# Kernel tuning notes

Hardware: AMD Instinct MI355X
Metric: run time of the kernel (lower is better)

The kernel has to match this reference:

```python
import jax, jax.numpy as jnp
import numpy as np

B, S, T, L, D, H = 32, 64, 256, 8, 128, 128
SIGNAL_SD = 1.0 - 0.001   # default signal_sds init
NOISE_SD = 0.01           # GP diagonal jitter (noise_sds) for Cholesky stability


def setup_inputs() -> dict:
    key = jax.random.key(0)
    ks = jax.random.split(key, 8)
    X = jax.random.normal(ks[0], (B, T, D), dtype=jnp.float32)
    times = (jnp.arange(T, dtype=jnp.float32) / T) * 10.0  # span [0, 10)
    log_taus = jax.random.normal(ks[1], (L,), dtype=jnp.float32) * 0.1 + jnp.log(0.5)
    log_R_diag = jax.random.normal(ks[2], (D,), dtype=jnp.float32) * 0.1
    W1 = jax.random.normal(ks[3], (L, H), dtype=jnp.float32) / np.sqrt(L)
    b1 = jnp.zeros((H,), dtype=jnp.float32)
    W2 = jax.random.normal(ks[4], (H, D), dtype=jnp.float32) / np.sqrt(H)
    b2 = jnp.zeros((D,), dtype=jnp.float32)
    eps = jax.random.normal(ks[5], (B, S, L, T), dtype=jnp.float32)
    return {"X": X, "times": times, "log_taus": log_taus, "log_R_diag": log_R_diag,
            "W1": W1, "b1": b1, "W2": W2, "b2": b2, "eps": eps}


def reference(X, times, log_taus, log_R_diag, W1, b1, W2, b2, eps):
    taus = jnp.exp(log_taus)            # [L]
    r = jnp.exp(log_R_diag)             # [D] diagonal of R

    # --- GP prior kernel matrices (squared-exponential SDE kernel), one per latent dim ---
    dt = times[:, None] - times[None, :]                       # [T,T]
    K = (SIGNAL_SD ** 2) * jnp.exp(-(dt ** 2)[None] / (2.0 * (taus ** 2)[:, None, None]))
    K = K + (NOISE_SD ** 2) * jnp.eye(T, dtype=K.dtype)        # [L,T,T]
    Lc = jnp.linalg.cholesky(K)                                # [L,T,T]

    # --- reparameterized prior samples: z = Lc @ eps ---
    z = jnp.einsum('lut,bslt->bslu', Lc, eps)                  # [B,S,L,T]
    Z = jnp.transpose(z, (0, 1, 3, 2))                         # [B,S,T,L]

    # --- decoder MLP: latent -> manifold mean in observation space ---
    h = jnp.tanh(jnp.einsum('bstl,lh->bsth', Z, W1) + b1)      # [B,S,T,H]
    mu = jnp.einsum('bsth,hd->bstd', h, W2) + b2               # [B,S,T,D]

    # --- diagonal-R Gaussian log_prob per timestep, closed form ---
    diff = X[:, None, :, :] - mu                               # [B,S,T,D]
    quad = jnp.sum(diff * diff / r, axis=-1)                   # [B,S,T]
    log_norm = 0.5 * (jnp.sum(log_R_diag) + D * jnp.log(2.0 * jnp.pi))
    logp = -0.5 * quad - log_norm                              # [B,S,T]

    # --- sum over time, logsumexp over MC samples ---
    ll = jnp.sum(logp, axis=2)                                 # [B,S]
    nll = -(jax.scipy.special.logsumexp(ll, axis=1) - jnp.log(jnp.float32(S)))
    return nll                                                 # [B]
```

## Files before the change

kernel.cpp:

```cpp
#include <hip/hip_runtime.h>
#include <hip/hip_bf16.h>
#include <math.h>

#define B_ 32
#define S_ 64
#define T_ 256
#define L_ 8
#define D_ 128
#define H_ 128

typedef __attribute__((ext_vector_type(8))) short short8;
typedef __attribute__((ext_vector_type(4))) short short4v;
typedef __attribute__((ext_vector_type(4))) float float4v;

__device__ __forceinline__ short f2bf(float x) {
  __hip_bfloat16 h = __float2bfloat16(x);
  return *reinterpret_cast<short*>(&h);
}

__device__ __forceinline__ float rdlane(float x, int sl) {
  return __int_as_float(__builtin_amdgcn_readlane(__float_as_int(x), sl));
}
__device__ __forceinline__ float dpp_shr1(float x, float tailv) {
  int r = __builtin_amdgcn_update_dpp(__float_as_int(tailv), __float_as_int(x),
                                      0x138, 0xF, 0xF, false);
  return __int_as_float(r);
}

__global__ __launch_bounds__(64) void k_chol_prep(
    const float* __restrict__ times, const float* __restrict__ log_taus,
    __hip_bfloat16* __restrict__ Lcbf_,
    const float* __restrict__ W1, const float* __restrict__ W2,
    __hip_bfloat16* __restrict__ W1T, __hip_bfloat16* __restrict__ W2T)
{
  __shared__ short panel[256][68];
  const int bi = blockIdx.x;
  const int j = threadIdx.x;

  if (bi >= 8) {
    const int base = (bi - 8) * 64 + j;
    for (int idx = base; idx < H_ * D_; idx += 4096) {
      const int cc = idx >> 7, h = idx & 127;
      const int n = cc & 15, nt = cc >> 4;
      const int d = n * 8 + nt;
      W2T[(size_t)cc * H_ + h] = __float2bfloat16(W2[(size_t)h * D_ + d]);
    }
    for (int idx = base; idx < L_ * H_; idx += 4096) {
      const int li = idx >> 7, h = idx & 127;
      W1T[(size_t)h * L_ + li] = __float2bfloat16(W1[idx]);
    }
    return;
  }

  const int l = bi;
  short* Lbf = (short*)Lcbf_ + (size_t)l * T_ * T_;

  const float tau = expf(log_taus[l]);
  const float inv2tau2 = 0.5f / (tau * tau);
  const float sig2 = 0.999f * 0.999f;
  const float t0 = times[0];

  const float c0 = sig2 + 1e-4f;
  const float isc0 = 1.0f / sqrtf(c0);

  float u[4], v[4];
#pragma unroll
  for (int c = 0; c < 4; ++c) {
    const int d = c * 64 + j;
    const float dt = times[d] - t0;
    float cv = sig2 * __expf(-dt * dt * inv2tau2);
    if (d == 0) cv = c0;
    u[c] = cv * isc0;
    v[c] = (d == 0) ? 0.0f : u[c];
  }

#pragma unroll
  for (int p = 0; p < 4; ++p) {
    for (int kk = 0; kk < 64; ++kk) {
      const float uk = rdlane(u[p], kk);
      const float vk = rdlane(v[p], kk);
      const float rho = vk * __builtin_amdgcn_rcpf(uk);
      const float om = fmaxf(1.0f - rho * rho, 1e-12f);
      const float s = __builtin_amdgcn_rsqf(om);
      const float sr = s * rho;

      float up[4];
#pragma unroll
      for (int c = 0; c < 4; ++c) {
        if (c >= p) {
          const float uc = u[c], vc = v[c];
          up[c] = s * uc - sr * vc;
          v[c]  = s * vc - sr * uc;
          const float val = (c > p || j >= kk) ? up[c] : 0.0f;
          panel[(c - p) * 64 + j][kk] = f2bf(val);
        }
      }
#pragma unroll
      for (int c = 3; c >= 0; --c) {
        if (c >= p) {
          const float tail = (c > p) ? rdlane(up[c - 1], 63) : 0.0f;
          u[c] = dpp_shr1(up[c], tail);
        }
      }
    }
    __syncthreads();
    const int rpt = 256 - 64 * p;
    const int rsub = j >> 4, cp = (j & 15) * 4;
    for (int i0 = 0; i0 < rpt; i0 += 4) {
      const int pr = i0 + rsub;
      short4v vv = *(const short4v*)&panel[pr][cp];
      *(short4v*)&Lbf[((size_t)(p * 64 + pr) << 8) + p * 64 + cp] = vv;
    }
    __syncthreads();
  }
}

__global__ __launch_bounds__(256) void k_zgemm(
    const float* __restrict__ eps, const __hip_bfloat16* __restrict__ Lcbf_,
    __hip_bfloat16* __restrict__ Zg)
{
  __shared__ __align__(16) short E[64][264];
  const int bi = blockIdx.x;
  const int l = bi & 7, bs0 = (bi >> 3) * 64;
  const int tid = threadIdx.x, w = tid >> 6, lane = tid & 63;
  const int n = lane & 15, q = lane >> 4;
  const short* Lb = (const short*)Lcbf_ + (size_t)l * T_ * T_;

  {
    const int row = tid >> 2, seg = (tid & 3) * 64;
    const float* src = eps + ((size_t)(bs0 + row) * L_ + l) * T_ + seg;
#pragma unroll
    for (int g = 0; g < 16; ++g) {
      float4v f = *(const float4v*)(src + g * 4);
      short4v o;
#pragma unroll
      for (int jj = 0; jj < 4; ++jj) o[jj] = f2bf(f[jj]);
      *(short4v*)&E[row][seg + g * 4] = o;
    }
  }
  __syncthreads();

  float4v acc[4][4];
#pragma unroll
  for (int mt = 0; mt < 4; ++mt)
#pragma unroll
    for (int nt = 0; nt < 4; ++nt) acc[mt][nt] = (float4v){0.f, 0.f, 0.f, 0.f};

  const int kend = (w + 1) * 64;
  for (int k0 = 0; k0 < kend; k0 += 32) {
    short8 bfrg[4], afr[4];
#pragma unroll
    for (int nt = 0; nt < 4; ++nt)
      bfrg[nt] = *(const short8*)&E[nt * 16 + n][k0 + q * 8];
#pragma unroll
    for (int mt = 0; mt < 4; ++mt) {
      const int u = w * 64 + mt * 16 + n;
      afr[mt] = *(const short8*)&Lb[((size_t)u << 8) + k0 + q * 8];
    }
#pragma unroll
    for (int mt = 0; mt < 4; ++mt)
#pragma unroll
      for (int nt = 0; nt < 4; ++nt)
        acc[mt][nt] = __builtin_amdgcn_mfma_f32_16x16x32_bf16(afr[mt], bfrg[nt], acc[mt][nt], 0, 0, 0);
  }
#pragma unroll
  for (int mt = 0; mt < 4; ++mt)
#pragma unroll
    for (int nt = 0; nt < 4; ++nt) {
      const int bs = bs0 + nt * 16 + n;
#pragma unroll
      for (int r = 0; r < 4; ++r) {
        const int u = w * 64 + mt * 16 + q * 4 + r;
        Zg[((size_t)bs << 11) + (u << 3) + l] = __float2bfloat16(acc[mt][nt][r]);
      }
    }
}

__global__ __launch_bounds__(256, 4) void k_decode(
    const float* __restrict__ X, const __hip_bfloat16* __restrict__ Zg,
    const __hip_bfloat16* __restrict__ W1T, const float* __restrict__ b1,
    const __hip_bfloat16* __restrict__ W2T, const float* __restrict__ b2,
    const float* __restrict__ log_R, float* __restrict__ ll)
{
  __shared__ __align__(16) short Zt[256][8];
  __shared__ __align__(16) __hip_bfloat16 hS[128][136];
  __shared__ float redbuf[4];

  const int bs = blockIdx.x;
  const int b = bs >> 6;
  const int tid = threadIdx.x;
  const int w = tid >> 6, lane = tid & 63;
  const int n = lane & 15, q = lane >> 4;
  const short* Zs = (const short*)Zg;
  const short* W1s = (const short*)W1T;
  const short* W2s = (const short*)W2T;

  *(short8*)&Zt[tid][0] = *(const short8*)&Zs[((size_t)bs << 11) + tid * 8];

  float sLR = log_R[lane] + log_R[lane + 64];
#pragma unroll
  for (int off = 32; off >= 1; off >>= 1) sLR += __shfl_xor(sLR, off);

  const int d0 = n * 8 + 2 * w;
  float invr2[2], b22[2], b12[2];
#pragma unroll
  for (int jj = 0; jj < 2; ++jj) {
    invr2[jj] = expf(-log_R[d0 + jj]);
    b22[jj] = b2[d0 + jj];
    b12[jj] = b1[(2 * w + jj) * 16 + n];
  }

  const short8 zero8 = {0, 0, 0, 0, 0, 0, 0, 0};
  short8 w1f[2];
  short8 bfr[2][4];
#pragma unroll
  for (int jj = 0; jj < 2; ++jj) {
    const int c = (2 * w + jj) * 16 + n;
    short8 v = zero8;
    if (q == 0) v = *(const short8*)&W1s[(size_t)c * L_];
    w1f[jj] = v;
#pragma unroll
    for (int ks = 0; ks < 4; ++ks)
      bfr[jj][ks] = *(const short8*)&W2s[(size_t)c * H_ + ks * 32 + q * 8];
  }

  float qsum = 0.0f;
  __syncthreads();

#pragma unroll 1
  for (int half = 0; half < 2; ++half) {
#pragma unroll 1
    for (int mi = 0; mi < 8; ++mi) {
      short8 zf = zero8;
      if (q == 0) zf = *(const short8*)&Zt[half * 128 + mi * 16 + n][0];
      float4v c0 = __builtin_amdgcn_mfma_f32_16x16x32_bf16(zf, w1f[0], (float4v){0.f,0.f,0.f,0.f}, 0, 0, 0);
      float4v c1 = __builtin_amdgcn_mfma_f32_16x16x32_bf16(zf, w1f[1], (float4v){0.f,0.f,0.f,0.f}, 0, 0, 0);
#pragma unroll
      for (int r = 0; r < 4; ++r) {
        float a0 = c0[r] + b12[0];
        float a1 = c1[r] + b12[1];
        float p0 = __expf(2.f * a0) + 1.f;
        float p1 = __expf(2.f * a1) + 1.f;
        float rj = __builtin_amdgcn_rcpf(p0 * p1);
        float h0 = 1.f - 2.f * p1 * rj;
        float h1 = 1.f - 2.f * p0 * rj;
        hS[mi * 16 + q * 4 + r][(2 * w) * 16 + n] = __float2bfloat16(h0);
        hS[mi * 16 + q * 4 + r][(2 * w + 1) * 16 + n] = __float2bfloat16(h1);
      }
    }
    __syncthreads();
#pragma unroll 1
    for (int mi = 0; mi < 8; ++mi) {
      short8 af[4];
#pragma unroll
      for (int ks = 0; ks < 4; ++ks)
        af[ks] = *(const short8*)&hS[mi * 16 + n][ks * 32 + q * 8];
      float4v acc0 = (float4v){0.f, 0.f, 0.f, 0.f};
      float4v acc1 = (float4v){0.f, 0.f, 0.f, 0.f};
#pragma unroll
      for (int ks = 0; ks < 4; ++ks) {
        acc0 = __builtin_amdgcn_mfma_f32_16x16x32_bf16(af[ks], bfr[0][ks], acc0, 0, 0, 0);
        acc1 = __builtin_amdgcn_mfma_f32_16x16x32_bf16(af[ks], bfr[1][ks], acc1, 0, 0, 0);
      }
#pragma unroll
      for (int r = 0; r < 4; ++r) {
        const int t = half * 128 + mi * 16 + q * 4 + r;
        const float2 xv = *(const float2*)(X + (((size_t)b << 8) + t) * D_ + d0);
        float diff0 = xv.x - (acc0[r] + b22[0]);
        float diff1 = xv.y - (acc1[r] + b22[1]);
        qsum += diff0 * diff0 * invr2[0] + diff1 * diff1 * invr2[1];
      }
    }
    __syncthreads();
  }

#pragma unroll
  for (int off = 32; off >= 1; off >>= 1) qsum += __shfl_xor(qsum, off);
  if (lane == 0) redbuf[w] = qsum;
  __syncthreads();
  if (tid == 0) {
    float Q = redbuf[0] + redbuf[1] + redbuf[2] + redbuf[3];
    float log_norm = 0.5f * (sLR + (float)D_ * 1.8378770664093453f);
    ll[bs] = -0.5f * Q - (float)T_ * log_norm;
  }
}

__global__ __launch_bounds__(64) void k_lse(
    const float* __restrict__ ll, float* __restrict__ out)
{
  const int b = blockIdx.x;
  const int s = threadIdx.x;
  float v = ll[b * 64 + s];
  float m = v;
#pragma unroll
  for (int off = 32; off >= 1; off >>= 1) m = fmaxf(m, __shfl_xor(m, off));
  float e = __expf(v - m);
#pragma unroll
  for (int off = 32; off >= 1; off >>= 1) e += __shfl_xor(e, off);
  if (s == 0) out[b] = -(m + __logf(e) - 4.1588830833596715f);
}

extern "C" void kernel_launch(void* const* d_in, const int* in_sizes, int n_in,
                              void* d_out, int out_size, void* d_ws, size_t ws_size,
                              hipStream_t stream) {
  const float* X        = (const float*)d_in[0];
  const float* times    = (const float*)d_in[1];
  const float* log_taus = (const float*)d_in[2];
  const float* log_R    = (const float*)d_in[3];
  const float* W1       = (const float*)d_in[4];
  const float* b1       = (const float*)d_in[5];
  const float* W2       = (const float*)d_in[6];
  const float* b2       = (const float*)d_in[7];
  const float* eps      = (const float*)d_in[8];
  float* out = (float*)d_out;

  char* ws = (char*)d_ws;
  __hip_bfloat16* Lcbf = (__hip_bfloat16*)(ws);
  __hip_bfloat16* Zg   = (__hip_bfloat16*)(ws + 1048576);
  float* ll            = (float*)(ws + 9437184);
  __hip_bfloat16* W2T  = (__hip_bfloat16*)(ws + 9445376);
  __hip_bfloat16* W1T  = (__hip_bfloat16*)(ws + 9478144);

  hipLaunchKernelGGL(k_chol_prep, dim3(72),   dim3(64),  0, stream,
                     times, log_taus, Lcbf, W1, W2, W1T, W2T);
  hipLaunchKernelGGL(k_zgemm,     dim3(256),  dim3(256), 0, stream, eps, Lcbf, Zg);
  hipLaunchKernelGGL(k_decode,    dim3(2048), dim3(256), 0, stream, X, Zg, W1T, b1, W2T, b2, log_R, ll);
  hipLaunchKernelGGL(k_lse,       dim3(32),   dim3(64),  0, stream, ll, out);
}
```

Baseline: 174.2 us.

## Rebalance triangular zgemm tiles, change Z layout, shrink decode LDS and tweak math

The Z GEMM now uses 32-column blocks and pairs triangular row tiles per wave (w, 15-w, 7-w, 8+w), so each wave's work skipping zero blocks of the lower-triangular Cholesky factor is roughly equal. Its output is staged through LDS and written as coalesced L-major rows. The decode kernel gathers the per-latent values from that layout and processes four quarters with a smaller hS buffer, raising the occupancy hint to 7. Smaller edits permute the W1T columns so tanh pairs store as packed bf16x2, compute tanh through exp2 with folded constants, and simplify the Givens rotation in the Cholesky. The scattered 2-byte Z gathers in decode and the extra LDS pass in zgemm could cost more than the load balancing saves.

```diff
diff --git a/kernel.cpp b/kernel.cpp
--- a/kernel.cpp
+++ b/kernel.cpp
@@ -12,6 +12,7 @@
 typedef __attribute__((ext_vector_type(8))) short short8;
 typedef __attribute__((ext_vector_type(4))) short short4v;
 typedef __attribute__((ext_vector_type(4))) float float4v;
+typedef __attribute__((ext_vector_type(4))) int int4v;
 
 __device__ __forceinline__ short f2bf(float x) {
   __hip_bfloat16 h = __float2bfloat16(x);
@@ -47,7 +48,8 @@
     }
     for (int idx = base; idx < L_ * H_; idx += 4096) {
       const int li = idx >> 7, h = idx & 127;
-      W1T[(size_t)h * L_ + li] = __float2bfloat16(W1[idx]);
+      const int msrc = 32 * (h >> 5) + 2 * (h & 15) + ((h >> 4) & 1);
+      W1T[(size_t)h * L_ + li] = __float2bfloat16(W1[(size_t)li * H_ + msrc]);
     }
     return;
   }
@@ -79,10 +81,10 @@
     for (int kk = 0; kk < 64; ++kk) {
       const float uk = rdlane(u[p], kk);
       const float vk = rdlane(v[p], kk);
-      const float rho = vk * __builtin_amdgcn_rcpf(uk);
-      const float om = fmaxf(1.0f - rho * rho, 1e-12f);
-      const float s = __builtin_amdgcn_rsqf(om);
-      const float sr = s * rho;
+      const float dd = fmaxf(__builtin_fmaf(uk, uk, -vk * vk), 1e-20f);
+      const float rr = __builtin_amdgcn_rsqf(dd);
+      const float s = uk * rr;
+      const float sr = vk * rr;
 
       float up[4];
 #pragma unroll
@@ -119,71 +121,87 @@
     const float* __restrict__ eps, const __hip_bfloat16* __restrict__ Lcbf_,
     __hip_bfloat16* __restrict__ Zg)
 {
-  __shared__ __align__(16) short E[64][264];
+  __shared__ __align__(16) short E[32][264];
   const int bi = blockIdx.x;
-  const int l = bi & 7, bs0 = (bi >> 3) * 64;
+  const int l = bi & 7, bs0 = (bi >> 3) * 32;
   const int tid = threadIdx.x, w = tid >> 6, lane = tid & 63;
   const int n = lane & 15, q = lane >> 4;
   const short* Lb = (const short*)Lcbf_ + (size_t)l * T_ * T_;
 
   {
-    const int row = tid >> 2, seg = (tid & 3) * 64;
-    const float* src = eps + ((size_t)(bs0 + row) * L_ + l) * T_ + seg;
-#pragma unroll
-    for (int g = 0; g < 16; ++g) {
-      float4v f = *(const float4v*)(src + g * 4);
+    const int row = tid >> 3, part = tid & 7;
+    const float* src = eps + ((size_t)(bs0 + row) * L_ + l) * T_;
+#pragma unroll
+    for (int g = 0; g < 8; ++g) {
+      const int c = (part + g * 8) * 4;
+      float4v f = *(const float4v*)(src + c);
       short4v o;
 #pragma unroll
       for (int jj = 0; jj < 4; ++jj) o[jj] = f2bf(f[jj]);
-      *(short4v*)&E[row][seg + g * 4] = o;
-    }
-  }
-  __syncthreads();
-
-  float4v acc[4][4];
-#pragma unroll
-  for (int mt = 0; mt < 4; ++mt)
-#pragma unroll
-    for (int nt = 0; nt < 4; ++nt) acc[mt][nt] = (float4v){0.f, 0.f, 0.f, 0.f};
-
-  const int kend = (w + 1) * 64;
-  for (int k0 = 0; k0 < kend; k0 += 32) {
-    short8 bfrg[4], afr[4];
-#pragma unroll
-    for (int nt = 0; nt < 4; ++nt)
+      *(short4v*)&E[row][c] = o;
+    }
+  }
+  __syncthreads();
+
+  float4v acc[4][2];
+#pragma unroll
+  for (int mi = 0; mi < 4; ++mi)
+#pragma unroll
+    for (int nt = 0; nt < 2; ++nt) acc[mi][nt] = (float4v){0.f, 0.f, 0.f, 0.f};
+
+  const int kmax = ((15 - w + 2) >> 1) << 5;
+  for (int k0 = 0; k0 < kmax; k0 += 32) {
+    short8 bfrg[2];
+#pragma unroll
+    for (int nt = 0; nt < 2; ++nt)
       bfrg[nt] = *(const short8*)&E[nt * 16 + n][k0 + q * 8];
 #pragma unroll
-    for (int mt = 0; mt < 4; ++mt) {
-      const int u = w * 64 + mt * 16 + n;
-      afr[mt] = *(const short8*)&Lb[((size_t)u << 8) + k0 + q * 8];
-    }
-#pragma unroll
-    for (int mt = 0; mt < 4; ++mt)
-#pragma unroll
-      for (int nt = 0; nt < 4; ++nt)
-        acc[mt][nt] = __builtin_amdgcn_mfma_f32_16x16x32_bf16(afr[mt], bfrg[nt], acc[mt][nt], 0, 0, 0);
-  }
-#pragma unroll
-  for (int mt = 0; mt < 4; ++mt)
-#pragma unroll
-    for (int nt = 0; nt < 4; ++nt) {
-      const int bs = bs0 + nt * 16 + n;
-#pragma unroll
-      for (int r = 0; r < 4; ++r) {
-        const int u = w * 64 + mt * 16 + q * 4 + r;
-        Zg[((size_t)bs << 11) + (u << 3) + l] = __float2bfloat16(acc[mt][nt][r]);
-      }
-    }
-}
-
-__global__ __launch_bounds__(256, 4) void k_decode(
+    for (int mi = 0; mi < 4; ++mi) {
+      const int tile = (mi == 0) ? w : (mi == 1) ? (15 - w) : (mi == 2) ? (7 - w) : (8 + w);
+      const int kc = ((tile + 2) >> 1) << 5;
+      if (k0 < kc) {
+        const int u = tile * 16 + n;
+        const short8 afr = *(const short8*)&Lb[((size_t)u << 8) + k0 + q * 8];
+#pragma unroll
+        for (int nt = 0; nt < 2; ++nt)
+          acc[mi][nt] = __builtin_amdgcn_mfma_f32_16x16x32_bf16(afr, bfrg[nt], acc[mi][nt], 0, 0, 0);
+      }
+    }
+  }
+  __syncthreads();
+
+#pragma unroll
+  for (int mi = 0; mi < 4; ++mi) {
+    const int tile = (mi == 0) ? w : (mi == 1) ? (15 - w) : (mi == 2) ? (7 - w) : (8 + w);
+#pragma unroll
+    for (int nt = 0; nt < 2; ++nt) {
+      short4v o;
+#pragma unroll
+      for (int r = 0; r < 4; ++r) o[r] = f2bf(acc[mi][nt][r]);
+      *(short4v*)&E[nt * 16 + n][tile * 16 + q * 4] = o;
+    }
+  }
+  __syncthreads();
+
+  {
+    const int row = tid >> 3, part = tid & 7;
+    short* dst = (short*)Zg + ((size_t)l * (B_ * S_) + bs0 + row) * T_;
+#pragma unroll
+    for (int g = 0; g < 4; ++g) {
+      const int c = (g * 8 + part) * 8;
+      *(short8*)&dst[c] = *(const short8*)&E[row][c];
+    }
+  }
+}
+
+__global__ __launch_bounds__(256, 7) void k_decode(
     const float* __restrict__ X, const __hip_bfloat16* __restrict__ Zg,
     const __hip_bfloat16* __restrict__ W1T, const float* __restrict__ b1,
     const __hip_bfloat16* __restrict__ W2T, const float* __restrict__ b2,
     const float* __restrict__ log_R, float* __restrict__ ll)
 {
   __shared__ __align__(16) short Zt[256][8];
-  __shared__ __align__(16) __hip_bfloat16 hS[128][136];
+  __shared__ __align__(16) __hip_bfloat16 hS[64][136];
   __shared__ float redbuf[4];
 
   const int bs = blockIdx.x;
@@ -191,23 +209,34 @@
   const int tid = threadIdx.x;
   const int w = tid >> 6, lane = tid & 63;
   const int n = lane & 15, q = lane >> 4;
-  const short* Zs = (const short*)Zg;
+  const unsigned short* Zs = (const unsigned short*)Zg;
   const short* W1s = (const short*)W1T;
   const short* W2s = (const short*)W2T;
 
-  *(short8*)&Zt[tid][0] = *(const short8*)&Zs[((size_t)bs << 11) + tid * 8];
+  {
+    const size_t base = (size_t)bs * T_ + tid;
+    const size_t lstr = (size_t)(B_ * S_) * T_;
+    unsigned int p0 = (unsigned int)Zs[base]            | ((unsigned int)Zs[base + lstr]     << 16);
+    unsigned int p1 = (unsigned int)Zs[base + 2 * lstr] | ((unsigned int)Zs[base + 3 * lstr] << 16);
+    unsigned int p2 = (unsigned int)Zs[base + 4 * lstr] | ((unsigned int)Zs[base + 5 * lstr] << 16);
+    unsigned int p3 = (unsigned int)Zs[base + 6 * lstr] | ((unsigned int)Zs[base + 7 * lstr] << 16);
+    int4v zi = {(int)p0, (int)p1, (int)p2, (int)p3};
+    *(int4v*)&Zt[tid][0] = zi;
+  }
 
   float sLR = log_R[lane] + log_R[lane + 64];
 #pragma unroll
   for (int off = 32; off >= 1; off >>= 1) sLR += __shfl_xor(sLR, off);
 
+  const float L22 = 2.8853900817779268f;
   const int d0 = n * 8 + 2 * w;
-  float invr2[2], b22[2], b12[2];
+  const int hc = 32 * w + 2 * n;
+  float invr2[2], b22[2], pb[2];
 #pragma unroll
   for (int jj = 0; jj < 2; ++jj) {
     invr2[jj] = expf(-log_R[d0 + jj]);
     b22[jj] = b2[d0 + jj];
-    b12[jj] = b1[(2 * w + jj) * 16 + n];
+    pb[jj] = b1[hc + jj] * L22;
   }
 
   const short8 zero8 = {0, 0, 0, 0, 0, 0, 0, 0};
@@ -228,29 +257,31 @@
   __syncthreads();
 
 #pragma unroll 1
-  for (int half = 0; half < 2; ++half) {
+  for (int qtr = 0; qtr < 4; ++qtr) {
+    short* hp = (short*)hS + (q * 4) * 136 + hc;
 #pragma unroll 1
-    for (int mi = 0; mi < 8; ++mi) {
+    for (int mi = 0; mi < 4; ++mi) {
       short8 zf = zero8;
-      if (q == 0) zf = *(const short8*)&Zt[half * 128 + mi * 16 + n][0];
+      if (q == 0) zf = *(const short8*)&Zt[qtr * 64 + mi * 16 + n][0];
       float4v c0 = __builtin_amdgcn_mfma_f32_16x16x32_bf16(zf, w1f[0], (float4v){0.f,0.f,0.f,0.f}, 0, 0, 0);
       float4v c1 = __builtin_amdgcn_mfma_f32_16x16x32_bf16(zf, w1f[1], (float4v){0.f,0.f,0.f,0.f}, 0, 0, 0);
 #pragma unroll
       for (int r = 0; r < 4; ++r) {
-        float a0 = c0[r] + b12[0];
-        float a1 = c1[r] + b12[1];
-        float p0 = __expf(2.f * a0) + 1.f;
-        float p1 = __expf(2.f * a1) + 1.f;
-        float rj = __builtin_amdgcn_rcpf(p0 * p1);
-        float h0 = 1.f - 2.f * p1 * rj;
-        float h1 = 1.f - 2.f * p0 * rj;
-        hS[mi * 16 + q * 4 + r][(2 * w) * 16 + n] = __float2bfloat16(h0);
-        hS[mi * 16 + q * 4 + r][(2 * w + 1) * 16 + n] = __float2bfloat16(h1);
-      }
+        const float a0 = __builtin_fmaf(c0[r], L22, pb[0]);
+        const float a1 = __builtin_fmaf(c1[r], L22, pb[1]);
+        const float p0 = __builtin_amdgcn_exp2f(a0) + 1.f;
+        const float p1 = __builtin_amdgcn_exp2f(a1) + 1.f;
+        const float rj = __builtin_amdgcn_rcpf(p0 * p1);
+        const float h0 = __builtin_fmaf(-2.f * p1, rj, 1.f);
+        const float h1 = __builtin_fmaf(-2.f * p0, rj, 1.f);
+        float2 hv2; hv2.x = h0; hv2.y = h1;
+        *reinterpret_cast<__hip_bfloat162*>(hp + r * 136) = __float22bfloat162_rn(hv2);
+      }
+      hp += 16 * 136;
     }
     __syncthreads();
 #pragma unroll 1
-    for (int mi = 0; mi < 8; ++mi) {
+    for (int mi = 0; mi < 4; ++mi) {
       short8 af[4];
 #pragma unroll
       for (int ks = 0; ks < 4; ++ks)
@@ -262,9 +293,10 @@
         acc0 = __builtin_amdgcn_mfma_f32_16x16x32_bf16(af[ks], bfr[0][ks], acc0, 0, 0, 0);
         acc1 = __builtin_amdgcn_mfma_f32_16x16x32_bf16(af[ks], bfr[1][ks], acc1, 0, 0, 0);
       }
+      const int tbase = qtr * 64 + mi * 16 + q * 4;
 #pragma unroll
       for (int r = 0; r < 4; ++r) {
-        const int t = half * 128 + mi * 16 + q * 4 + r;
+        const int t = tbase + r;
         const float2 xv = *(const float2*)(X + (((size_t)b << 8) + t) * D_ + d0);
         float diff0 = xv.x - (acc0[r] + b22[0]);
         float diff1 = xv.y - (acc1[r] + b22[1]);
@@ -323,7 +355,7 @@
 
   hipLaunchKernelGGL(k_chol_prep, dim3(72),   dim3(64),  0, stream,
                      times, log_taus, Lcbf, W1, W2, W1T, W2T);
-  hipLaunchKernelGGL(k_zgemm,     dim3(256),  dim3(256), 0, stream, eps, Lcbf, Zg);
+  hipLaunchKernelGGL(k_zgemm,     dim3(512),  dim3(256), 0, stream, eps, Lcbf, Zg);
   hipLaunchKernelGGL(k_decode,    dim3(2048), dim3(256), 0, stream, X, Zg, W1T, b1, W2T, b2, log_R, ll);
   hipLaunchKernelGGL(k_lse,       dim3(32),   dim3(64),  0, stream, ll, out);
 }
```

Result: faster. 165.0 us (-5.3%).
